# Kernel optimization log

Hardware: AMD Instinct MI355X
Metric: run time of the kernel (lower is better)

The kernel has to match this reference:

```python
import jax, jax.numpy as jnp
import numpy as np

# Module hyperparameters (from init_kwargs)
LATENT = 1024
H = 16          # num query heads
HK = 4          # num key/value heads (GQA)
D = 64          # head_dim
CAUSAL = True
QKV_OUT = (3 * H + 2 * HK) * D  # 3584, as defined in the source module


def setup_inputs() -> dict:
    key = jax.random.key(0)
    k1, k2, k3 = jax.random.split(key, 3)
    B, S = 2, 2048
    x = jax.random.normal(k1, (B, S, LATENT), dtype=jnp.float32)
    # nn.Linear weights are [out_features, in_features]; scale like torch default init
    w_qkv = jax.random.normal(k2, (QKV_OUT, LATENT), dtype=jnp.float32) / np.sqrt(LATENT)
    w_out = jax.random.normal(k3, (LATENT, H * D), dtype=jnp.float32) / np.sqrt(H * D)
    return {"x": x, "w_qkv": w_qkv, "w_out": w_out}


def reference(x, w_qkv, w_out):
    B, S, _ = x.shape
    scale = 1.0 / np.sqrt(D).astype(np.float32)

    # Fused QKV projection: [B,S,(3H+2HK)*D]
    qkv = jnp.einsum('bsl,ol->bso', x, w_qkv)

    # Split: q takes H heads, k and v take HK heads each (GQA).
    # (The extra 2*H*D columns of the fused projection are allocated by the
    #  source module but unused by q/k/v, matching its layer sizing.)
    q = qkv[..., : H * D].reshape(B, S, H, D)
    k = qkv[..., H * D:(H + HK) * D].reshape(B, S, HK, D)
    v = qkv[..., (H + HK) * D:(H + 2 * HK) * D].reshape(B, S, HK, D)

    # Expand KV heads to match query heads (group factor H // HK)
    rep = H // HK
    k = jnp.repeat(k, rep, axis=2)  # [B,S,H,D]
    v = jnp.repeat(v, rep, axis=2)

    # Scaled dot-product attention
    scores = jnp.einsum('bshd,bthd->bhst', q, k) * scale  # [B,H,S,S]
    if CAUSAL:
        causal_mask = jnp.tril(jnp.ones((S, S), dtype=bool))
        scores = jnp.where(causal_mask, scores, jnp.finfo(scores.dtype).min)
    attn = jax.nn.softmax(scores, axis=-1)
    out = jnp.einsum('bhst,bthd->bshd', attn, v).reshape(B, S, H * D)

    # Output projection back to latent_size
    return jnp.einsum('bso,lo->bsl', out, w_out)
```

## Files before the change

kernel.cpp:

```cpp
#include <hip/hip_runtime.h>
#include <hip/hip_bf16.h>
#include <math.h>

typedef __attribute__((ext_vector_type(8))) short bf16x8;
typedef __attribute__((ext_vector_type(4))) float f32x4;
typedef unsigned short u16;
typedef unsigned int   u32;

#define DEVINL __device__ __forceinline__

DEVINL u16 f2bf(float x) {
    u32 u = __float_as_uint(x);
    u += 0x7fffu + ((u >> 16) & 1u);
    return (u16)(u >> 16);
}

DEVINL void gl_lds16(const void* g, void* s) {
    __builtin_amdgcn_global_load_lds(
        (const __attribute__((address_space(1))) u32*)g,
        (__attribute__((address_space(3))) u32*)s,
        16, 0, 0);
}

DEVINL f32x4 mfma16(bf16x8 a, bf16x8 b, f32x4 c) {
    return __builtin_amdgcn_mfma_f32_16x16x32_bf16(a, b, c, 0, 0, 0);
}

__global__ void cvt3(const float* __restrict__ x, const float* __restrict__ wq,
                     const float* __restrict__ wo,
                     u16* __restrict__ xb, u16* __restrict__ wqb, u16* __restrict__ wob) {
    int i = blockIdx.x * 256 + threadIdx.x;
    const float* s; u16* d; int j;
    if (i < 1048576)      { s = x;  d = xb;  j = i; }
    else if (i < 1441792) { s = wq; d = wqb; j = i - 1048576; }
    else                  { s = wo; d = wob; j = i - 1441792; }
    float4 v = ((const float4*)s)[j];
    ushort4 o;
    o.x = f2bf(v.x); o.y = f2bf(v.y); o.z = f2bf(v.z); o.w = f2bf(v.w);
    ((ushort4*)d)[j] = o;
}

template<int BN, int EP>
__launch_bounds__(256)
__global__ void gemm_rp(const u16* __restrict__ A, const u16* __restrict__ B,
                        const int N, const int K,
                        float* __restrict__ Cf,
                        u16* __restrict__ Qo, u16* __restrict__ Ko, u16* __restrict__ Vo)
{
    constexpr int NB = BN / 32;
    __shared__ __align__(16) u16 As[2][64 * 64];
    __shared__ __align__(16) u16 Bs[2][BN * 64];
    const int tid  = threadIdx.x;
    const int lane = tid & 63;
    const int quad = lane >> 4;
    const int lcol = lane & 15;
    const int w    = tid >> 6;
    const int wr   = w >> 1, wc = w & 1;
    const int lr   = lane >> 3;
    const int lc   = lane & 7;
    const int swst = lc ^ lr;
    const int rk   = lcol & 7;

    const int nwg = gridDim.x * gridDim.y;
    int bid = blockIdx.y * gridDim.x + blockIdx.x;
    bid = (bid & 7) * (nwg >> 3) + (bid >> 3);
    const int m0 = (bid / gridDim.x) * 64;
    const int n0 = (bid % gridDim.x) * BN;

    f32x4 acc[2][NB];
    for (int mb = 0; mb < 2; mb++)
        for (int nb = 0; nb < NB; nb++)
            for (int i = 0; i < 4; i++) acc[mb][nb][i] = 0.f;

    const u16* Ap = A + (m0 + w * 16 + lr) * K + swst * 8;
    const u16* Bp = B + (n0 + w * (BN / 4) + lr) * K + swst * 8;

    for (int j = 0; j < 2; j++)
        gl_lds16(Ap + j * 8 * K, &As[0][(w * 16 + j * 8) * 64]);
    for (int g = 0; g < NB; g++)
        gl_lds16(Bp + g * 8 * K, &Bs[0][(w * (BN / 4) + g * 8) * 64]);
    __syncthreads();

    int cur = 0;
    for (int k0 = 0; k0 < K; k0 += 64) {
        if (k0 + 64 < K) {
            for (int j = 0; j < 2; j++)
                gl_lds16(Ap + j * 8 * K + k0 + 64, &As[cur ^ 1][(w * 16 + j * 8) * 64]);
            for (int g = 0; g < NB; g++)
                gl_lds16(Bp + g * 8 * K + k0 + 64, &Bs[cur ^ 1][(w * (BN / 4) + g * 8) * 64]);
        }
        bf16x8 af[2][2], bfv[NB][2];
        for (int ks = 0; ks < 2; ks++) {
            const int ch = ((ks * 4 + quad) ^ rk) * 8;
            for (int mb = 0; mb < 2; mb++)
                af[mb][ks] = *(const bf16x8*)&As[cur][(wr * 32 + mb * 16 + lcol) * 64 + ch];
            for (int nb = 0; nb < NB; nb++)
                bfv[nb][ks] = *(const bf16x8*)&Bs[cur][(wc * (BN / 2) + nb * 16 + lcol) * 64 + ch];
        }
        for (int ks = 0; ks < 2; ks++)
            for (int mb = 0; mb < 2; mb++)
                for (int nb = 0; nb < NB; nb++)
                    acc[mb][nb] = mfma16(af[mb][ks], bfv[nb][ks], acc[mb][nb]);
        __syncthreads();
        cur ^= 1;
    }

    if (EP == 0) {
        for (int mb = 0; mb < 2; mb++)
            for (int nb = 0; nb < NB; nb++) {
                int row = m0 + wr * 32 + mb * 16 + quad * 4;
                int col = n0 + wc * (BN / 2) + nb * 16 + lcol;
                for (int i = 0; i < 4; i++)
                    Cf[(row + i) * N + col] = acc[mb][nb][i];
            }
    } else {
        const float qsc = 0.18033688011112042f;
        for (int mb = 0; mb < 2; mb++)
            for (int nb = 0; nb < NB; nb++)
                for (int i = 0; i < 4; i++) {
                    int row = m0 + wr * 32 + mb * 16 + quad * 4 + i;
                    int col = n0 + wc * (BN / 2) + nb * 16 + lcol;
                    int bb = row >> 11, ss = row & 2047;
                    if (col < 1024) {
                        int hh = col >> 6, dd = col & 63;
                        Qo[((bb * 16 + hh) * 2048 + ss) * 64 + dd] = f2bf(acc[mb][nb][i] * qsc);
                    } else if (col < 1280) {
                        int c = col - 1024, hh = c >> 6, dd = c & 63;
                        Ko[((bb * 4 + hh) * 2048 + ss) * 64 + dd] = f2bf(acc[mb][nb][i]);
                    } else {
                        int c = col - 1280, hh = c >> 6, dd = c & 63;
                        Vo[((bb * 4 + hh) * 64 + dd) * 2048 + ss] = f2bf(acc[mb][nb][i]);
                    }
                }
    }
}

__launch_bounds__(512, 4)
__global__ void attn_kernel(const u16* __restrict__ Qg, const u16* __restrict__ Kg,
                            const u16* __restrict__ Vtg, u16* __restrict__ Og)
{
    __shared__ __align__(16) u16 Ks[2][2][64 * 64];
    __shared__ __align__(16) u16 Vs[2][2][64 * 64];
    __shared__ __align__(16) u16 Ps[2][64 * 64];

    const int tid  = threadIdx.x;
    const int lane = tid & 63;
    const int w8   = tid >> 6;
    const int gpp  = w8 >> 2;
    const int wg   = w8 & 3;
    const int quad = lane >> 4;
    const int lcol = lane & 15;
    const int lr   = lane >> 3;
    const int lc   = lane & 7;
    const int swst = lc ^ lr;
    const int rk   = lcol & 7;
    const int hl   = lcol >> 3;

    const int p  = blockIdx.x;
    const int h  = blockIdx.y;
    const int b  = blockIdx.z;
    const int hk = h >> 2;

    const u16* Qp = Qg  + (b * 16 + h) * 2048 * 64;
    const u16* Kp = Kg  + (b * 4 + hk) * 2048 * 64;
    const u16* Vp = Vtg + (b * 4 + hk) * 64 * 2048;

    const int p0 = (wg * 16 + quad * 4) * 64 + ((hl ^ ((quad & 1) << 2)) << 3) + lc;

    float* Ob = (float*)(&Ks[1][0][0]);
    float* Lb = (float*)(&Vs[1][0][0]);

    for (int pass = 0; pass < 2; pass++) {
        const int qi = pass ? (31 - p) : p;
        const int q0 = qi * 64;
        const int nt = qi + 1;
        const int nIter = (nt + 1) >> 1;

        bf16x8 aqr[2];
        for (int ks = 0; ks < 2; ks++)
            aqr[ks] = *(const bf16x8*)(Qp + (q0 + wg * 16 + lcol) * 64 + ks * 32 + quad * 8);

        if (gpp < nt) {
            for (int j = 0; j < 2; j++) {
                const int r = wg * 16 + j * 8 + lr;
                gl_lds16(Kp + (gpp * 64 + r) * 64 + swst * 8, &Ks[gpp][0][wg * 1024 + j * 512]);
                gl_lds16(Vp + r * 2048 + gpp * 64 + swst * 8, &Vs[gpp][0][wg * 1024 + j * 512]);
            }
        }

        f32x4 o[4];
        float l_p[4];
        for (int db = 0; db < 4; db++)
            for (int i = 0; i < 4; i++) o[db][i] = 0.f;
        for (int i = 0; i < 4; i++) l_p[i] = 0.f;

        __syncthreads();

        for (int it = 0; it < nIter; ++it) {
            const int cur = it & 1;
            const int ti  = 2 * it + gpp;
            const int tin = ti + 2;
            if (tin < nt) {
                const int nbuf = cur ^ 1;
                for (int j = 0; j < 2; j++) {
                    const int r = wg * 16 + j * 8 + lr;
                    gl_lds16(Kp + (tin * 64 + r) * 64 + swst * 8, &Ks[gpp][nbuf][wg * 1024 + j * 512]);
                    gl_lds16(Vp + r * 2048 + tin * 64 + swst * 8, &Vs[gpp][nbuf][wg * 1024 + j * 512]);
                }
            }
            if (ti < nt) {
                f32x4 s[4];
                for (int cb = 0; cb < 4; cb++)
                    for (int i = 0; i < 4; i++) s[cb][i] = 0.f;
                __builtin_amdgcn_s_setprio(1);
                for (int ks = 0; ks < 2; ks++) {
                    const int chq = ((ks * 4 + quad) ^ rk) * 8;
                    for (int cb = 0; cb < 4; cb++) {
                        bf16x8 bk = *(const bf16x8*)&Ks[gpp][cur][(cb * 16 + lcol) * 64 + chq];
                        s[cb] = mfma16(aqr[ks], bk, s[cb]);
                    }
                }
                __builtin_amdgcn_s_setprio(0);

                if (ti == nt - 1) {
                    for (int cb = 0; cb < 4; cb++)
                        for (int i = 0; i < 4; i++) {
                            const bool masked = (cb * 16 + lcol) > (wg * 16 + quad * 4 + i);
                            s[cb][i] = masked ? -INFINITY : s[cb][i];
                        }
                }

                for (int cb = 0; cb < 4; cb++)
                    for (int i = 0; i < 4; i++) {
                        const float pv = __builtin_amdgcn_exp2f(s[cb][i]);
                        s[cb][i] = pv;
                        l_p[i] += pv;
                    }

                for (int cb = 0; cb < 4; cb++)
                    for (int i = 0; i < 4; i++)
                        Ps[gpp][(p0 + i * 64) ^ (((cb * 2) ^ i) << 3)] =
                            (u16)(__float_as_uint(s[cb][i]) >> 16);

                __builtin_amdgcn_s_setprio(1);
                for (int kt = 0; kt < 2; kt++) {
                    const int chp = ((kt * 4 + quad) ^ rk) * 8;
                    bf16x8 ap = *(const bf16x8*)&Ps[gpp][(wg * 16 + lcol) * 64 + chp];
                    for (int db = 0; db < 4; db++) {
                        bf16x8 bv = *(const bf16x8*)&Vs[gpp][cur][(db * 16 + lcol) * 64 + chp];
                        o[db] = mfma16(ap, bv, o[db]);
                    }
                }
                __builtin_amdgcn_s_setprio(0);
            }
            __syncthreads();
        }

        float lrow[4];
        for (int i = 0; i < 4; i++) {
            float l = l_p[i];
            for (int x = 1; x < 16; x <<= 1) l += __shfl_xor(l, x);
            lrow[i] = l;
        }
        if (gpp == 1) {
            for (int i = 0; i < 4; i++) {
                const int row = wg * 16 + quad * 4 + i;
                for (int db = 0; db < 4; db++)
                    Ob[row * 64 + db * 16 + lcol] = o[db][i];
                if (lcol == 0) Lb[row] = lrow[i];
            }
        }
        __syncthreads();
        if (gpp == 0) {
            for (int i = 0; i < 4; i++) {
                const int row = wg * 16 + quad * 4 + i;
                const float inv = 1.0f / (lrow[i] + Lb[row]);
                const int srow = q0 + row;
                for (int db = 0; db < 4; db++) {
                    const float val = (o[db][i] + Ob[row * 64 + db * 16 + lcol]) * inv;
                    Og[(b * 2048 + srow) * 1024 + h * 64 + db * 16 + lcol] = f2bf(val);
                }
            }
        }
        __syncthreads();
    }
}

extern "C" void kernel_launch(void* const* d_in, const int* in_sizes, int n_in,
                              void* d_out, int out_size, void* d_ws, size_t ws_size,
                              hipStream_t stream) {
    const float* x     = (const float*)d_in[0];
    const float* w_qkv = (const float*)d_in[1];
    const float* w_out = (const float*)d_in[2];
    float* out = (float*)d_out;
    char* ws = (char*)d_ws;

    u16* xb  = (u16*)(ws);
    u16* wqb = (u16*)(ws + 8  * 1024 * 1024);
    u16* wob = (u16*)(ws + 11 * 1024 * 1024);
    u16* qb  = (u16*)(ws + 13 * 1024 * 1024);
    u16* kb  = (u16*)(ws + 21 * 1024 * 1024);
    u16* vtb = (u16*)(ws + 23 * 1024 * 1024);
    u16* aob = (u16*)(ws);

    cvt3<<<6656, 256, 0, stream>>>(x, w_qkv, w_out, xb, wqb, wob);

    gemm_rp<128, 1><<<dim3(12, 64), 256, 0, stream>>>(xb, wqb, 1536, 1024,
                                                      nullptr, qb, kb, vtb);
    attn_kernel<<<dim3(16, 16, 2), 512, 0, stream>>>(qb, kb, vtb, aob);
    gemm_rp<128, 0><<<dim3(8, 64), 256, 0, stream>>>(aob, wob, 1024, 1024,
                                                     out, nullptr, nullptr, nullptr);
}
```

Before: 152.7 us.

## Load V fragments directly from global into registers instead of LDS staging

Drops the shared-memory double buffer for V. Each wave now loads its V MFMA operands straight from global memory into registers, issuing them before the QK MFMAs so the latency is hidden, with scheduling barriers to hold that order. This frees LDS and removes the LDS write/read traffic for V, which may raise occupancy. In exchange, the four waves sharing a KV tile each re-read V from global/L2 instead of sharing one LDS copy, and register pressure goes up.

```diff
diff --git a/kernel.cpp b/kernel.cpp
--- a/kernel.cpp
+++ b/kernel.cpp
@@ -140,8 +140,8 @@
                             const u16* __restrict__ Vtg, u16* __restrict__ Og)
 {
     __shared__ __align__(16) u16 Ks[2][2][64 * 64];
-    __shared__ __align__(16) u16 Vs[2][2][64 * 64];
     __shared__ __align__(16) u16 Ps[2][64 * 64];
+    __shared__ float Lb[64];
 
     const int tid  = threadIdx.x;
     const int lane = tid & 63;
@@ -168,7 +168,6 @@
     const int p0 = (wg * 16 + quad * 4) * 64 + ((hl ^ ((quad & 1) << 2)) << 3) + lc;
 
     float* Ob = (float*)(&Ks[1][0][0]);
-    float* Lb = (float*)(&Vs[1][0][0]);
 
     for (int pass = 0; pass < 2; pass++) {
         const int qi = pass ? (31 - p) : p;
@@ -184,7 +183,6 @@
             for (int j = 0; j < 2; j++) {
                 const int r = wg * 16 + j * 8 + lr;
                 gl_lds16(Kp + (gpp * 64 + r) * 64 + swst * 8, &Ks[gpp][0][wg * 1024 + j * 512]);
-                gl_lds16(Vp + r * 2048 + gpp * 64 + swst * 8, &Vs[gpp][0][wg * 1024 + j * 512]);
             }
         }
 
@@ -205,10 +203,16 @@
                 for (int j = 0; j < 2; j++) {
                     const int r = wg * 16 + j * 8 + lr;
                     gl_lds16(Kp + (tin * 64 + r) * 64 + swst * 8, &Ks[gpp][nbuf][wg * 1024 + j * 512]);
-                    gl_lds16(Vp + r * 2048 + tin * 64 + swst * 8, &Vs[gpp][nbuf][wg * 1024 + j * 512]);
                 }
             }
             if (ti < nt) {
+                const u16* Vt = Vp + ti * 64;
+
+                bf16x8 bv0[4];
+                for (int db = 0; db < 4; db++)
+                    bv0[db] = *(const bf16x8*)(Vt + (db * 16 + lcol) * 2048 + quad * 8);
+                __builtin_amdgcn_sched_barrier(0);
+
                 f32x4 s[4];
                 for (int cb = 0; cb < 4; cb++)
                     for (int i = 0; i < 4; i++) s[cb][i] = 0.f;
@@ -222,6 +226,11 @@
                 }
                 __builtin_amdgcn_s_setprio(0);
 
+                bf16x8 bv1[4];
+                for (int db = 0; db < 4; db++)
+                    bv1[db] = *(const bf16x8*)(Vt + (db * 16 + lcol) * 2048 + 32 + quad * 8);
+                __builtin_amdgcn_sched_barrier(0);
+
                 if (ti == nt - 1) {
                     for (int cb = 0; cb < 4; cb++)
                         for (int i = 0; i < 4; i++) {
@@ -243,13 +252,17 @@
                             (u16)(__float_as_uint(s[cb][i]) >> 16);
 
                 __builtin_amdgcn_s_setprio(1);
-                for (int kt = 0; kt < 2; kt++) {
-                    const int chp = ((kt * 4 + quad) ^ rk) * 8;
-                    bf16x8 ap = *(const bf16x8*)&Ps[gpp][(wg * 16 + lcol) * 64 + chp];
-                    for (int db = 0; db < 4; db++) {
-                        bf16x8 bv = *(const bf16x8*)&Vs[gpp][cur][(db * 16 + lcol) * 64 + chp];
-                        o[db] = mfma16(ap, bv, o[db]);
-                    }
+                {
+                    const int chp0 = ((0 * 4 + quad) ^ rk) * 8;
+                    bf16x8 ap = *(const bf16x8*)&Ps[gpp][(wg * 16 + lcol) * 64 + chp0];
+                    for (int db = 0; db < 4; db++)
+                        o[db] = mfma16(ap, bv0[db], o[db]);
+                }
+                {
+                    const int chp1 = ((1 * 4 + quad) ^ rk) * 8;
+                    bf16x8 ap = *(const bf16x8*)&Ps[gpp][(wg * 16 + lcol) * 64 + chp1];
+                    for (int db = 0; db < 4; db++)
+                        o[db] = mfma16(ap, bv1[db], o[db]);
                 }
                 __builtin_amdgcn_s_setprio(0);
             }
```

Result: slower. 187.7 us (+22.9%).
